# Performance work log

Hardware: AMD Instinct MI355X
Metric: run time of the kernel (lower is better)

Reference implementation:

```python
import jax, jax.numpy as jnp
import numpy as np

IN_DIM, UNITS, OUT_DIM = 128, 256, 8
DENSITY = 0.5  # 1 - sparsity_level
B, T = 256, 512


def _ncp_dims():
    Nm = OUT_DIM
    Nc = max(int(0.4 * (UNITS - Nm)), 1)   # command neurons (AutoNCP rule)
    Ni = UNITS - Nm - Nc                    # inter neurons
    return Ni, Nc, Nm


def _fanout_mask(rng, n_src, n_dst, fanout):
    # each source connects to `fanout` distinct random destinations
    idx = np.argsort(rng.random((n_src, n_dst)), axis=1)[:, :fanout]
    m = np.zeros((n_src, n_dst), dtype=np.int32)
    m[np.arange(n_src)[:, None], idx] = 1
    return m


def setup_inputs() -> dict:
    key = jax.random.key(0)
    rng = np.random.default_rng(22222)
    Ni, Nc, Nm = _ncp_dims()
    s_fan = max(int(Ni * DENSITY), 1)       # sensory fanout
    i_fan = max(int(Nc * DENSITY), 1)       # inter fanout
    m_fanin = max(int(Nc * DENSITY), 1)     # motor fanin
    M_si = _fanout_mask(rng, IN_DIM, Ni, s_fan)      # sensory -> inter
    M_ic = _fanout_mask(rng, Ni, Nc, i_fan)          # inter -> command
    M_cm = _fanout_mask(rng, Nm, Nc, m_fanin).T      # command -> motor (fanin per motor)

    def layer_mask(M_in, hid):
        # WiredCfCCell: concat input sparsity with dense ones for the recurrent block, then transpose
        return np.concatenate([M_in, np.ones((hid, hid), np.int32)], axis=0).T

    masks = [layer_mask(M_si, Ni), layer_mask(M_ic, Nc), layer_mask(M_cm, Nm)]
    dims = [(IN_DIM, Ni), (Ni, Nc), (Nc, Nm)]
    inp = {}
    for l, (fin, hid) in enumerate(dims):
        cat = fin + hid
        scale = 1.0 / np.sqrt(cat)
        for nm in ("w1", "w2", "wa", "wb"):
            inp[f"{nm}_{l}"] = jnp.asarray(rng.normal(0.0, scale, (hid, cat)).astype(np.float32))
        for nm in ("b1", "b2", "ba", "bb"):
            inp[f"{nm}_{l}"] = jnp.zeros((hid,), jnp.float32)
        inp[f"m{l}"] = jnp.asarray(masks[l])  # int32, constant sparsity mask
    k1, k2 = jax.random.split(key)
    inp["x"] = jax.random.normal(k1, (B, T, IN_DIM), jnp.float32)
    inp["dt"] = jax.random.uniform(k2, (1,), jnp.float32, 0.5, 1.5)
    return inp


def _cfc_cell(xh, w1, b1, w2, b2, wa, ba, wb, bb, m, ts):
    # CfCCell, mode='default', no backbone, sparsity mask on ff1/ff2 weights
    mf = m.astype(w1.dtype)
    ff1 = jnp.tanh(xh @ (w1 * mf).T + b1)
    ff2 = jnp.tanh(xh @ (w2 * mf).T + b2)
    t_interp = jax.nn.sigmoid((xh @ wa.T + ba) * ts + (xh @ wb.T + bb))
    return ff1 * (1.0 - t_interp) + t_interp * ff2


def _forward(x, dt, params, masks):
    Ni, Nc, Nm = _ncp_dims()
    ts = dt[0]
    h0 = jnp.zeros((x.shape[0], Ni), x.dtype)
    h1 = jnp.zeros((x.shape[0], Nc), x.dtype)
    h2 = jnp.zeros((x.shape[0], Nm), x.dtype)
    p0, p1, p2 = params

    def step(carry, xt):
        h0, h1, h2 = carry
        nh0 = _cfc_cell(jnp.concatenate([xt, h0], 1), *p0, masks[0], ts)
        nh1 = _cfc_cell(jnp.concatenate([nh0, h1], 1), *p1, masks[1], ts)
        nh2 = _cfc_cell(jnp.concatenate([nh1, h2], 1), *p2, masks[2], ts)
        return (nh0, nh1, nh2), nh2

    (h0, h1, h2), ys = jax.lax.scan(step, (h0, h1, h2), jnp.swapaxes(x, 0, 1))
    y = jnp.tanh(jnp.swapaxes(ys, 0, 1))          # (B, T, OUT_DIM), tanh output saturation
    h_out = jnp.concatenate([h0, h1, h2], axis=1)  # (B, units)
    return y, h_out


def reference(x, dt,
              w1_0, b1_0, w2_0, b2_0, wa_0, ba_0, wb_0, bb_0, m0,
              w1_1, b1_1, w2_1, b2_1, wa_1, ba_1, wb_1, bb_1, m1,
              w1_2, b1_2, w2_2, b2_2, wa_2, ba_2, wb_2, bb_2, m2):
    params = ((w1_0, b1_0, w2_0, b2_0, wa_0, ba_0, wb_0, bb_0),
              (w1_1, b1_1, w2_1, b2_1, wa_1, ba_1, wb_1, bb_1),
              (w1_2, b1_2, w2_2, b2_2, wa_2, ba_2, wb_2, bb_2))
    return _forward(x, dt, params, (m0, m1, m2))
```

## Files before the change

kernel.cpp:

```cpp
#include <hip/hip_runtime.h>
#include <cmath>


typedef _Float16 f16;
typedef f16 h4 __attribute__((ext_vector_type(4)));
typedef f16 h8 __attribute__((ext_vector_type(8)));
typedef float f4 __attribute__((ext_vector_type(4)));

#define MFMA(a, b, c) __builtin_amdgcn_mfma_f32_16x16x32_f16(a, b, c, 0, 0, 0)
#define RAW_BAR() asm volatile("s_waitcnt lgkmcnt(0)\n\ts_barrier" ::: "memory")

constexpr int IN_DIM = 128, Ni = 149, Nc = 99, Nm = 8;
constexpr int CAT0 = 277, CAT1 = 248, CAT2 = 107;
constexpr int Bsz = 256, Tsz = 512;
constexpr int TC = 64, NCH = 8, NBT = 16;
constexpr int NSUB = NCH * 4;
constexpr int NT0 = 30, NT1 = 21;
constexpr int S0 = 168, S2 = 136;
constexpr int NXWG1 = 64;
constexpr int NXWG0 = 128;
constexpr size_t XU0C = (size_t)TC * NBT * NT0 * 256;
constexpr size_t NH0C = (size_t)TC * NBT * 2560;
constexpr size_t XU1C = (size_t)TC * NBT * NT1 * 256;
constexpr size_t H0S_HALVES = (size_t)NBT * 16 * S0;
constexpr size_t H12S_HALVES = (size_t)NBT * 2 * 16 * S2;
constexpr size_t YOFF = (size_t)Bsz * Tsz * 8;
constexpr float L2E = 1.4426950408889634f;

constexpr int OFF_X0 = 0;
constexpr int OFF_R0 = 7680;
constexpr int OFF_X1 = 17280;
constexpr int OFF_R12A = 24000;
constexpr int OFF_R12B = 29376;
constexpr int NFRAG = 30144;

constexpr int CSTRIDE = 16;
constexpr int C_X0 = 0, C_R0S = 8, C_X1S = 40, C_R12S = 72;
constexpr int NCNT = 104 * CSTRIDE;

__device__ inline float rcpf_(float x) { return __builtin_amdgcn_rcpf(x); }
__device__ __forceinline__ float exp2p_(float x) {
#if __has_builtin(__builtin_amdgcn_exp2f)
  return __builtin_amdgcn_exp2f(x);
#else
  return exp2f(x);
#endif
}
__device__ __forceinline__ float cfc_h(float a0, float a1, float a2) {
  float e0 = exp2p_(a0), e1 = exp2p_(a1), e2 = exp2p_(a2);
  float pa = 1.f + e0, ma = 1.f - e0;
  float pb = 1.f + e1, mb = 1.f - e1;
  float pc = 1.f + e2;
  float num = fmaf(ma * pb, e2, mb * pa);
  return num * rcpf_(pa * pb * pc);
}
__device__ __forceinline__ float tanhp_(float x) {
  float e = exp2p_(-2.f * L2E * x);
  return (1.f - e) * rcpf_(1.f + e);
}

__device__ __forceinline__ void spin_relaxed(int* p, int target) {
  if (threadIdx.x == 0) {
    long it = 0;
    while (__hip_atomic_load(p, __ATOMIC_RELAXED, __HIP_MEMORY_SCOPE_AGENT) <
               target &&
           ++it < (1L << 22))
      __builtin_amdgcn_s_sleep(4);
  }
  __syncthreads();
}
__device__ __forceinline__ void spin_acq(int* p, int target) {
  spin_relaxed(p, target);
  __builtin_amdgcn_fence(__ATOMIC_ACQUIRE, "agent");
}
__device__ __forceinline__ void sig_relaxed(int* p) {
  __syncthreads();
  if (threadIdx.x == 0)
    __hip_atomic_fetch_add(p, 1, __ATOMIC_RELAXED, __HIP_MEMORY_SCOPE_AGENT);
}
__device__ __forceinline__ void sig_rel(int* p) {
  __syncthreads();
  if (threadIdx.x == 0)
    __hip_atomic_fetch_add(p, 1, __ATOMIC_RELEASE, __HIP_MEMORY_SCOPE_AGENT);
}

__device__ __forceinline__ void store_short_sc(f16* p, f16 v) {
  unsigned u = (unsigned)__builtin_bit_cast(unsigned short, v);
  asm volatile("global_store_short %0, %1, off sc0 sc1" ::"v"(
                   (unsigned long long)p),
               "v"(u)
               : "memory");
}
__device__ __forceinline__ void load_A5_sc(const f16* base, h8 (&A)[5]) {
  unsigned long long b = (unsigned long long)base;
  asm volatile(
      "global_load_dwordx4 %0, %5, off sc0 sc1\n\t"
      "global_load_dwordx4 %1, %5, off offset:64 sc0 sc1\n\t"
      "global_load_dwordx4 %2, %5, off offset:128 sc0 sc1\n\t"
      "global_load_dwordx4 %3, %5, off offset:192 sc0 sc1\n\t"
      "global_load_dwordx4 %4, %5, off offset:256 sc0 sc1\n\t"
      "s_waitcnt vmcnt(0)"
      : "=&v"(A[0]), "=&v"(A[1]), "=&v"(A[2]), "=&v"(A[3]), "=&v"(A[4])
      : "v"(b)
      : "memory");
}

__global__ __launch_bounds__(256) void pack_kernel(
    const float* __restrict__ w1_0, const float* __restrict__ w2_0,
    const float* __restrict__ wa_0, const float* __restrict__ wb_0,
    const int* __restrict__ m0,
    const float* __restrict__ w1_1, const float* __restrict__ w2_1,
    const float* __restrict__ wa_1, const float* __restrict__ wb_1,
    const int* __restrict__ m1,
    const float* __restrict__ w1_2, const float* __restrict__ w2_2,
    const float* __restrict__ wa_2, const float* __restrict__ wb_2,
    const int* __restrict__ m2, const float* __restrict__ dtp,
    f16* __restrict__ PK, int* __restrict__ CNT) {
  if (blockIdx.x == 0)
    for (int i = threadIdx.x; i < NCNT; i += 256)
      __hip_atomic_store(&CNT[i], 0, __ATOMIC_RELAXED, __HIP_MEMORY_SCOPE_AGENT);
  int idx = blockIdx.x * 256 + threadIdx.x;
  if (idx >= NFRAG) return;
  int lane = idx & 63, col = lane & 15, q = lane >> 4;
  float ts = dtp[0];
  const float* Wa = nullptr;
  const float* Wb = nullptr;
  const int* M = nullptr;
  int ld, n, nmax, k0, kmax;
  int mat;
  if (idx < OFF_R0) {
    int p = idx >> 6;
    mat = p / 40; int nt = (p >> 2) % 10, kt = p & 3;
    ld = CAT0; n = nt * 16 + col; nmax = Ni; k0 = kt * 32 + q * 8; kmax = IN_DIM;
    if (mat == 0) { Wa = w1_0; M = m0; }
    else if (mat == 1) { Wa = w2_0; M = m0; }
    else { Wa = wa_0; Wb = wb_0; }
  } else if (idx < OFF_X1) {
    int p = (idx - OFF_R0) >> 6;
    int g = p / 15; mat = (p / 5) % 3; int kt = p % 5;
    ld = CAT0; n = g * 16 + col; nmax = Ni; k0 = IN_DIM + kt * 32 + q * 8; kmax = CAT0;
    if (mat == 0) Wa = w1_0;
    else if (mat == 1) Wa = w2_0;
    else { Wa = wa_0; Wb = wb_0; }
  } else if (idx < OFF_R12A) {
    int p = (idx - OFF_X1) >> 6;
    mat = p / 35; int nt = (p / 5) % 7, kt = p % 5;
    ld = CAT1; n = nt * 16 + col; nmax = Nc; k0 = kt * 32 + q * 8; kmax = Ni;
    if (mat == 0) { Wa = w1_1; M = m1; }
    else if (mat == 1) { Wa = w2_1; M = m1; }
    else { Wa = wa_1; Wb = wb_1; }
  } else if (idx < OFF_R12B) {
    int p = (idx - OFF_R12A) >> 6;
    int wv = p / 12; mat = (p / 4) % 3; int kt = p & 3;
    ld = CAT1; n = wv * 16 + col; nmax = Nc; k0 = Ni + kt * 32 + q * 8; kmax = CAT1;
    if (mat == 0) Wa = w1_1;
    else if (mat == 1) Wa = w2_1;
    else { Wa = wa_1; Wb = wb_1; }
  } else {
    int p = (idx - OFF_R12B) >> 6;
    mat = p / 4; int kt = p & 3;
    ld = CAT2; n = col; nmax = Nm; k0 = kt * 32 + q * 8; kmax = CAT2;
    if (mat == 0) { Wa = w1_2; M = m2; }
    else if (mat == 1) { Wa = w2_2; M = m2; }
    else { Wa = wa_2; Wb = wb_2; }
  }
  h8 r;
#pragma unroll
  for (int j = 0; j < 8; j++) {
    int k = k0 + j;
    float v = 0.f;
    if (n < nmax && k < kmax) {
      if (mat < 2) {
        v = Wa[(size_t)n * ld + k];
        if (M) v *= (float)M[(size_t)n * ld + k];
        v *= -2.f * L2E;
      } else {
        v = -L2E * (ts * Wa[(size_t)n * ld + k] + Wb[(size_t)n * ld + k]);
      }
    }
    r[j] = (f16)v;
  }
  ((h8*)PK)[idx] = r;
}

__device__ __forceinline__ void r0_step(
    const f16* br, f16* bw, const f16* __restrict__ XU0, f16* __restrict__ NH0,
    float* __restrict__ out, const h8 (&Bf)[3][5], h4 (&xu)[3],
    int t, int tload, int bt, int g, int lane, int col, int q, int n, bool last) {
  h8 A[5];
#pragma unroll
  for (int kt = 0; kt < 5; kt++)
    A[kt] = *(const h8*)(br + col * S0 + kt * 32 + q * 8);
  f4 acc0 = {(float)xu[0][0], (float)xu[0][1], (float)xu[0][2], (float)xu[0][3]};
  f4 acc1 = {(float)xu[1][0], (float)xu[1][1], (float)xu[1][2], (float)xu[1][3]};
  f4 acc2 = {(float)xu[2][0], (float)xu[2][1], (float)xu[2][2], (float)xu[2][3]};
  size_t mtl = (size_t)tload * NBT + bt;
#pragma unroll
  for (int mat = 0; mat < 3; mat++)
    xu[mat] = *(const h4*)(XU0 + (mtl * NT0 + mat * 10 + g) * 256 + lane * 4);
#pragma unroll
  for (int kt = 0; kt < 5; kt++) {
    acc0 = MFMA(A[kt], Bf[0][kt], acc0);
    acc1 = MFMA(A[kt], Bf[1][kt], acc1);
    acc2 = MFMA(A[kt], Bf[2][kt], acc2);
  }
  int mt = t * NBT + bt;
  f16* nh = NH0 + (size_t)mt * 2560;
#pragma unroll
  for (int r = 0; r < 4; r++) {
    int m = q * 4 + r;
    float h = cfc_h(acc0[r], acc1[r], acc2[r]);
    f16 h16 = (f16)h;
    bw[m * S0 + n] = h16;
    store_short_sc(nh + (size_t)m * 160 + n, h16);
    if (last && n < Ni) out[YOFF + (size_t)(bt * 16 + m) * 256 + n] = h;
  }
}

__device__ __forceinline__ void r12l1_step(
    const f16* br, f16* bw, const f16* __restrict__ XU1, float* __restrict__ out,
    const h8 (&Bf)[3][4], h4 (&xu)[3],
    int tload, int bt, int w, int lane, int col, int q, int n, bool last) {
  h8 A[4];
#pragma unroll
  for (int kt = 0; kt < 4; kt++)
    A[kt] = *(const h8*)(br + col * S2 + kt * 32 + q * 8);
  f4 acc0 = {(float)xu[0][0], (float)xu[0][1], (float)xu[0][2], (float)xu[0][3]};
  f4 acc1 = {(float)xu[1][0], (float)xu[1][1], (float)xu[1][2], (float)xu[1][3]};
  f4 acc2 = {(float)xu[2][0], (float)xu[2][1], (float)xu[2][2], (float)xu[2][3]};
  size_t mtl = (size_t)tload * NBT + bt;
#pragma unroll
  for (int mat = 0; mat < 3; mat++)
    xu[mat] = *(const h4*)(XU1 + (mtl * NT1 + mat * 7 + w) * 256 + lane * 4);
#pragma unroll
  for (int kt = 0; kt < 4; kt++) {
    acc0 = MFMA(A[kt], Bf[0][kt], acc0);
    acc1 = MFMA(A[kt], Bf[1][kt], acc1);
    acc2 = MFMA(A[kt], Bf[2][kt], acc2);
  }
#pragma unroll
  for (int r = 0; r < 4; r++) {
    int m = q * 4 + r;
    float h = cfc_h(acc0[r], acc1[r], acc2[r]);
    if (n < Nc) {
      bw[m * S2 + n] = (f16)h;
      if (last) out[YOFF + (size_t)(bt * 16 + m) * 256 + Ni + n] = h;
    }
  }
}

__device__ __forceinline__ void r12l2_step(
    const f16* rb, f16* wb, float* __restrict__ out, const h8 (&Bf)[3][4],
    float bn0, float bn1, float bn2, int tg, int bt, int col, int q, bool last) {
  h8 A[4];
#pragma unroll
  for (int kt = 0; kt < 4; kt++)
    A[kt] = *(const h8*)(rb + col * S2 + kt * 32 + q * 8);
  f4 acc0 = {bn0, bn0, bn0, bn0};
  f4 acc1 = {bn1, bn1, bn1, bn1};
  f4 acc2 = {bn2, bn2, bn2, bn2};
#pragma unroll
  for (int kt = 0; kt < 4; kt++) {
    acc0 = MFMA(A[kt], Bf[0][kt], acc0);
    acc1 = MFMA(A[kt], Bf[1][kt], acc1);
    acc2 = MFMA(A[kt], Bf[2][kt], acc2);
  }
#pragma unroll
  for (int r = 0; r < 4; r++) {
    int m = q * 4 + r;
    float h = cfc_h(acc0[r], acc1[r], acc2[r]);
    if (col < Nm) {
      out[((size_t)(bt * 16 + m) * Tsz + tg) * 8 + col] = tanhp_(h);
      wb[m * S2 + Nc + col] = (f16)h;
      if (last) out[YOFF + (size_t)(bt * 16 + m) * 256 + Ni + Nc + col] = h;
    }
  }
}

__global__ __launch_bounds__(640) void R_kernel(
    const h8* __restrict__ pk,
    const float* __restrict__ b1_0, const float* __restrict__ b2_0,
    const float* __restrict__ ba_0, const float* __restrict__ bb_0,
    const float* __restrict__ b1_1, const float* __restrict__ b2_1,
    const float* __restrict__ ba_1, const float* __restrict__ bb_1,
    const float* __restrict__ c1, const float* __restrict__ c2,
    const float* __restrict__ ca, const float* __restrict__ cb,
    const float* __restrict__ dtp, const float* __restrict__ x,
    f16* __restrict__ XU0, f16* __restrict__ NH0, f16* __restrict__ XU1,
    f16* __restrict__ H0S, f16* __restrict__ H12S,
    int* __restrict__ CNT, float* __restrict__ out, int c) {
  __shared__ __align__(16) char smem[10752];
  int tid = threadIdx.x;
  int g = tid >> 6, lane = tid & 63, col = lane & 15, q = lane >> 4;
  int wg = blockIdx.x;
  float ts = dtp[0];

  if (wg < NBT) {
    if (c < 0 || c >= NCH) return;
    spin_relaxed(&CNT[(C_X0 + c) * CSTRIDE], NXWG0);
    if (c >= 2)
      spin_relaxed(&CNT[(C_X1S + 4 * (c - 2) + 3) * CSTRIDE], NBT);
    const f16* XU0r = XU0 + (size_t)(c & 1) * XU0C;
    f16* NH0w = NH0 + (size_t)(c & 1) * NH0C;
    f16(*buf)[16 * S0] = (f16(*)[16 * S0])smem;
    int bt = wg;
    int n = g * 16 + col;
    h8 Bf[3][5];
#pragma unroll
    for (int mat = 0; mat < 3; mat++)
#pragma unroll
      for (int kt = 0; kt < 5; kt++)
        Bf[mat][kt] = pk[OFF_R0 + ((g * 3 + mat) * 5 + kt) * 64 + lane];

    for (int idx = tid; idx < 16 * S0; idx += 640) {
      buf[0][idx] = (c == 0) ? (f16)0.f : H0S[(size_t)bt * 16 * S0 + idx];
      buf[1][idx] = (f16)0.f;
    }
    __syncthreads();

    h4 xu0[3], xu1[3], xu2[3], xu3[3];
#pragma unroll
    for (int mat = 0; mat < 3; mat++) {
      xu0[mat] = *(const h4*)(XU0r + ((size_t)(0 * NBT + bt) * NT0 + mat * 10 + g) * 256 + lane * 4);
      xu1[mat] = *(const h4*)(XU0r + ((size_t)(1 * NBT + bt) * NT0 + mat * 10 + g) * 256 + lane * 4);
      xu2[mat] = *(const h4*)(XU0r + ((size_t)(2 * NBT + bt) * NT0 + mat * 10 + g) * 256 + lane * 4);
      xu3[mat] = *(const h4*)(XU0r + ((size_t)(3 * NBT + bt) * NT0 + mat * 10 + g) * 256 + lane * 4);
    }

    for (int t = 0; t < TC; t += 4) {
      r0_step(buf[0], buf[1], XU0r, NH0w, out, Bf, xu0, t, (t + 4 < TC) ? t + 4 : t,
              bt, g, lane, col, q, n, false);
      RAW_BAR();
      r0_step(buf[1], buf[0], XU0r, NH0w, out, Bf, xu1, t + 1,
              (t + 5 < TC) ? t + 5 : t + 1, bt, g, lane, col, q, n, false);
      RAW_BAR();
      r0_step(buf[0], buf[1], XU0r, NH0w, out, Bf, xu2, t + 2,
              (t + 6 < TC) ? t + 6 : t + 2, bt, g, lane, col, q, n, false);
      RAW_BAR();
      bool lastD = (c == NCH - 1) && (t + 3 == TC - 1);
      r0_step(buf[1], buf[0], XU0r, NH0w, out, Bf, xu3, t + 3,
              (t + 7 < TC) ? t + 7 : t + 3, bt, g, lane, col, q, n, lastD);
      RAW_BAR();
      if ((t & 12) == 12)
        sig_relaxed(&CNT[(C_R0S + 4 * c + (t >> 4)) * CSTRIDE]);
    }
    for (int idx = tid; idx < 16 * S0; idx += 640)
      H0S[(size_t)bt * 16 * S0 + idx] = buf[0][idx];

  } else if (wg < 2 * NBT) {
    int Glo = 4 * c - 2; if (Glo < 0) Glo = 0;
    int Ghi = 4 * c + 1; if (Ghi > NSUB - 1) Ghi = NSUB - 1;
    if (Glo > Ghi || c < 0) return;
    f16(*buf)[16 * S2] = (f16(*)[16 * S2])smem;
    int bt = wg - NBT;
    int w = g;
    int n = w * 16 + col;
    h8 Bf[3][4];
    float bn0 = 0.f, bn1 = 0.f, bn2 = 0.f;
    if (w < 7) {
#pragma unroll
      for (int mat = 0; mat < 3; mat++)
#pragma unroll
        for (int kt = 0; kt < 4; kt++)
          Bf[mat][kt] = pk[OFF_R12A + ((w * 3 + mat) * 4 + kt) * 64 + lane];
    } else if (w == 7) {
#pragma unroll
      for (int mat = 0; mat < 3; mat++)
#pragma unroll
        for (int kt = 0; kt < 4; kt++)
          Bf[mat][kt] = pk[OFF_R12B + (mat * 4 + kt) * 64 + lane];
      bn0 = (col < Nm) ? -2.f * L2E * c1[col] : 0.f;
      bn1 = (col < Nm) ? -2.f * L2E * c2[col] : 0.f;
      bn2 = (col < Nm) ? -L2E * (ts * ca[col] + cb[col]) : 0.f;
    }
    for (int idx = tid; idx < 2 * 16 * S2; idx += 640)
      ((f16*)buf)[idx] = (Glo == 0) ? (f16)0.f : H12S[(size_t)bt * 2 * 16 * S2 + idx];
    __syncthreads();

    for (int G = Glo; G <= Ghi; ++G) {
      int m = G >> 2, t0 = (G & 3) * 16;
      spin_acq(&CNT[(C_X1S + G) * CSTRIDE], NBT);
      const f16* XU1r = XU1 + (size_t)(m & 1) * XU1C;
      h4 xuA[3], xuB[3];
      if (w < 7) {
#pragma unroll
        for (int mat = 0; mat < 3; mat++) {
          xuA[mat] = *(const h4*)(XU1r + ((size_t)(t0 * NBT + bt) * NT1 + mat * 7 + w) * 256 + lane * 4);
          xuB[mat] = *(const h4*)(XU1r +
                                  ((size_t)((t0 + 1) * NBT + bt) * NT1 + mat * 7 + w) * 256 + lane * 4);
        }
      }
      for (int t = t0; t < t0 + 16; t += 2) {
        if (w < 7) {
          int tlA = (t + 2 < t0 + 16) ? t + 2 : t;
          r12l1_step(buf[0], buf[1], XU1r, out, Bf, xuA, tlA, bt, w, lane, col, q, n,
                     false);
        }
        RAW_BAR();
        if (w == 7)
          r12l2_step(buf[1], buf[0], out, Bf, bn0, bn1, bn2, m * TC + t, bt, col, q,
                     false);
        if (w < 7) {
          int tlB = (t + 3 < t0 + 16) ? t + 3 : t + 1;
          bool lastB = (m == NCH - 1) && (t + 1 == TC - 1);
          r12l1_step(buf[1], buf[0], XU1r, out, Bf, xuB, tlB, bt, w, lane, col, q, n,
                     lastB);
        }
        RAW_BAR();
        if (w == 7)
          r12l2_step(buf[0], buf[1], out, Bf, bn0, bn1, bn2, m * TC + t + 1, bt, col,
                     q, (m == NCH - 1) && (t + 1 == TC - 1));
      }
      sig_relaxed(&CNT[(C_R12S + G) * CSTRIDE]);
    }
    for (int idx = tid; idx < 2 * 16 * S2; idx += 640)
      H12S[(size_t)bt * 2 * 16 * S2 + idx] = ((f16*)buf)[idx];

  } else if (wg < 2 * NBT + NXWG1) {
    int bx = wg - 2 * NBT;
    int k = bx >> 4;
    int m = (k == 3) ? c - 1 : c;
    if (m < 0 || m >= NCH) return;
    int G = 4 * m + k;
    int w = g;
    int n = w * 16 + col;
    h8 Bf[3][5];
    float bias[3] = {0.f, 0.f, 0.f};
    if (w < 7) {
#pragma unroll
      for (int mat = 0; mat < 3; mat++)
#pragma unroll
        for (int kt = 0; kt < 5; kt++)
          Bf[mat][kt] = pk[OFF_X1 + (mat * 35 + w * 5 + kt) * 64 + lane];
      bias[0] = (n < Nc) ? -2.f * L2E * b1_1[n] : 0.f;
      bias[1] = (n < Nc) ? -2.f * L2E * b2_1[n] : 0.f;
      bias[2] = (n < Nc) ? -L2E * (ts * ba_1[n] + bb_1[n]) : 0.f;
    }
    spin_relaxed(&CNT[(C_R0S + G) * CSTRIDE], NBT);
    if (m >= 2)
      spin_relaxed(&CNT[(C_R12S + 4 * (m - 2) + 3) * CSTRIDE], NBT);
    const f16* NH0r = NH0 + (size_t)(m & 1) * NH0C;
    f16* XU1w = XU1 + (size_t)(m & 1) * XU1C;
    if (w < 7) {
      for (int i = 0; i < 16; i++) {
        int mt = bx * 16 + i;
        const f16* base = NH0r + (size_t)mt * 2560 + col * 160 + q * 8;
        h8 A[5];
        load_A5_sc(base, A);
#pragma unroll
        for (int mat = 0; mat < 3; mat++) {
          float b = bias[mat];
          f4 acc = {b, b, b, b};
#pragma unroll
          for (int kt = 0; kt < 5; kt++) acc = MFMA(A[kt], Bf[mat][kt], acc);
          h4 o;
#pragma unroll
          for (int rr = 0; rr < 4; rr++) o[rr] = (f16)acc[rr];
          *(h4*)(XU1w + ((size_t)mt * NT1 + mat * 7 + w) * 256 + lane * 4) = o;
        }
      }
    }
    sig_rel(&CNT[(C_X1S + G) * CSTRIDE]);

  } else {
    int cn = c + 1;
    if (cn >= NCH) return;
    if (cn >= 2)
      spin_relaxed(&CNT[(C_R0S + 4 * (cn - 2) + 3) * CSTRIDE], NBT);
    f16* XU0w = XU0 + (size_t)(cn & 1) * XU0C;
    f16* stg = (f16*)smem;
    int bx = wg - 2 * NBT - NXWG1;
    int w = g;
    int n = w * 16 + col;
    h8 Bx[3][4];
    float bias[3];
#pragma unroll
    for (int mat = 0; mat < 3; mat++)
#pragma unroll
      for (int kt = 0; kt < 4; kt++)
        Bx[mat][kt] = pk[OFF_X0 + ((mat * 10 + w) * 4 + kt) * 64 + lane];
    bias[0] = (n < Ni) ? -2.f * L2E * b1_0[n] : 0.f;
    bias[1] = (n < Ni) ? -2.f * L2E * b2_0[n] : 0.f;
    bias[2] = (n < Ni) ? -L2E * (ts * ba_0[n] + bb_0[n]) : 0.f;
    for (int i = 0; i < (TC * NBT) / NXWG0; i++) {
      int mt = bx * ((TC * NBT) / NXWG0) + i;
      int tl = mt >> 4, bt = mt & 15;
      int tg = cn * TC + tl;
      if (tid < 256) {
        int sr = tid >> 4, sc = (tid & 15) * 8;
        const float* xp = x + ((size_t)(bt * 16 + sr) * Tsz + tg) * IN_DIM + sc;
        h8 hv;
#pragma unroll
        for (int j = 0; j < 8; j++) hv[j] = (f16)xp[j];
        *(h8*)(stg + sr * 136 + sc) = hv;
      }
      __syncthreads();
      h8 A[4];
#pragma unroll
      for (int kt = 0; kt < 4; kt++)
        A[kt] = *(const h8*)(stg + col * 136 + kt * 32 + q * 8);
#pragma unroll
      for (int mat = 0; mat < 3; mat++) {
        float b = bias[mat];
        f4 acc = {b, b, b, b};
#pragma unroll
        for (int kt = 0; kt < 4; kt++) acc = MFMA(A[kt], Bx[mat][kt], acc);
        h4 o;
#pragma unroll
        for (int rr = 0; rr < 4; rr++) o[rr] = (f16)acc[rr];
        *(h4*)(XU0w + ((size_t)mt * NT0 + mat * 10 + w) * 256 + lane * 4) = o;
      }
      __syncthreads();
    }
    sig_relaxed(&CNT[(C_X0 + cn) * CSTRIDE]);
  }
}

extern "C" void kernel_launch(void* const* d_in, const int* in_sizes, int n_in,
                              void* d_out, int out_size, void* d_ws, size_t ws_size,
                              hipStream_t stream) {
  const float* w1_0 = (const float*)d_in[0];
  const float* w2_0 = (const float*)d_in[1];
  const float* wa_0 = (const float*)d_in[2];
  const float* wb_0 = (const float*)d_in[3];
  const float* b1_0 = (const float*)d_in[4];
  const float* b2_0 = (const float*)d_in[5];
  const float* ba_0 = (const float*)d_in[6];
  const float* bb_0 = (const float*)d_in[7];
  const int* m0 = (const int*)d_in[8];
  const float* w1_1 = (const float*)d_in[9];
  const float* w2_1 = (const float*)d_in[10];
  const float* wa_1 = (const float*)d_in[11];
  const float* wb_1 = (const float*)d_in[12];
  const float* b1_1 = (const float*)d_in[13];
  const float* b2_1 = (const float*)d_in[14];
  const float* ba_1 = (const float*)d_in[15];
  const float* bb_1 = (const float*)d_in[16];
  const int* m1 = (const int*)d_in[17];
  const float* w1_2 = (const float*)d_in[18];
  const float* w2_2 = (const float*)d_in[19];
  const float* wa_2 = (const float*)d_in[20];
  const float* wb_2 = (const float*)d_in[21];
  const float* c1 = (const float*)d_in[22];
  const float* c2 = (const float*)d_in[23];
  const float* ca = (const float*)d_in[24];
  const float* cb = (const float*)d_in[25];
  const int* m2 = (const int*)d_in[26];
  const float* x = (const float*)d_in[27];
  const float* dt = (const float*)d_in[28];
  float* out = (float*)d_out;

  f16* XU0 = (f16*)d_ws;
  f16* NH0 = XU0 + 2 * XU0C;
  f16* XU1 = NH0 + 2 * NH0C;
  f16* H0S = XU1 + 2 * XU1C;
  f16* H12S = H0S + H0S_HALVES;
  f16* PK = H12S + H12S_HALVES;
  int* CNT = (int*)(PK + (size_t)NFRAG * 8);
  const h8* pk = (const h8*)PK;

  hipMemsetAsync(CNT, 0, NCNT * sizeof(int), stream);

  pack_kernel<<<(NFRAG + 255) / 256, 256, 0, stream>>>(
      w1_0, w2_0, wa_0, wb_0, m0, w1_1, w2_1, wa_1, wb_1, m1,
      w1_2, w2_2, wa_2, wb_2, m2, dt, PK, CNT);

  for (int c = -1; c <= NCH; c++)
    R_kernel<<<2 * NBT + NXWG1 + NXWG0, 640, 0, stream>>>(
        pk, b1_0, b2_0, ba_0, bb_0, b1_1, b2_1, ba_1, bb_1,
        c1, c2, ca, cb, dt, x, XU0, NH0, XU1, H0S, H12S, CNT, out, c);
}
```

Before: 706.0 us.

## Fold weight packing into first R_kernel launch and drop trailing launch

Removes the separate pack_kernel launch by having the c==-1 launch of R_kernel pack weight fragments, synchronize all workgroups through a grid-wide counter, then compute chunk 0's input projection across all workgroups. The final c==NCH launch is removed by moving its remaining work (the last chunk's layer-1 input projection and recurrent tail) into the c==NCH-1 launch, with extra spin waits on existing counters. This cuts two kernel launches and spreads the first chunk's projection across more workgroups. It relies on all 240 workgroups being co-resident for the grid-wide spin, which could deadlock if occupancy doesn't allow it.

Result: slower. 725.4 us (+2.7%).

```diff
diff --git a/kernel.cpp b/kernel.cpp
--- a/kernel.cpp
+++ b/kernel.cpp
@@ -19,6 +19,7 @@
 constexpr int S0 = 168, S2 = 136;
 constexpr int NXWG1 = 64;
 constexpr int NXWG0 = 128;
+constexpr int NWGALL = 2 * NBT + NXWG1 + NXWG0;
 constexpr size_t XU0C = (size_t)TC * NBT * NT0 * 256;
 constexpr size_t NH0C = (size_t)TC * NBT * 2560;
 constexpr size_t XU1C = (size_t)TC * NBT * NT1 * 256;
@@ -35,8 +36,8 @@
 constexpr int NFRAG = 30144;
 
 constexpr int CSTRIDE = 16;
-constexpr int C_X0 = 0, C_R0S = 8, C_X1S = 40, C_R12S = 72;
-constexpr int NCNT = 104 * CSTRIDE;
+constexpr int C_X0 = 0, C_R0S = 8, C_X1S = 40, C_R12S = 72, C_PK = 104;
+constexpr int NCNT = 105 * CSTRIDE;
 
 __device__ inline float rcpf_(float x) { return __builtin_amdgcn_rcpf(x); }
 __device__ __forceinline__ float exp2p_(float x) {
@@ -105,7 +106,8 @@
       : "memory");
 }
 
-__global__ __launch_bounds__(256) void pack_kernel(
+__device__ __forceinline__ void pack_one(
+    int idx,
     const float* __restrict__ w1_0, const float* __restrict__ w2_0,
     const float* __restrict__ wa_0, const float* __restrict__ wb_0,
     const int* __restrict__ m0,
@@ -114,15 +116,8 @@
     const int* __restrict__ m1,
     const float* __restrict__ w1_2, const float* __restrict__ w2_2,
     const float* __restrict__ wa_2, const float* __restrict__ wb_2,
-    const int* __restrict__ m2, const float* __restrict__ dtp,
-    f16* __restrict__ PK, int* __restrict__ CNT) {
-  if (blockIdx.x == 0)
-    for (int i = threadIdx.x; i < NCNT; i += 256)
-      __hip_atomic_store(&CNT[i], 0, __ATOMIC_RELAXED, __HIP_MEMORY_SCOPE_AGENT);
-  int idx = blockIdx.x * 256 + threadIdx.x;
-  if (idx >= NFRAG) return;
+    const int* __restrict__ m2, float ts, f16* __restrict__ PK) {
   int lane = idx & 63, col = lane & 15, q = lane >> 4;
-  float ts = dtp[0];
   const float* Wa = nullptr;
   const float* Wb = nullptr;
   const int* M = nullptr;
@@ -278,7 +273,16 @@
 }
 
 __global__ __launch_bounds__(640) void R_kernel(
-    const h8* __restrict__ pk,
+    f16* __restrict__ PK,
+    const float* __restrict__ w1_0, const float* __restrict__ w2_0,
+    const float* __restrict__ wa_0, const float* __restrict__ wb_0,
+    const int* __restrict__ m0,
+    const float* __restrict__ w1_1, const float* __restrict__ w2_1,
+    const float* __restrict__ wa_1, const float* __restrict__ wb_1,
+    const int* __restrict__ m1,
+    const float* __restrict__ w1_2, const float* __restrict__ w2_2,
+    const float* __restrict__ wa_2, const float* __restrict__ wb_2,
+    const int* __restrict__ m2,
     const float* __restrict__ b1_0, const float* __restrict__ b2_0,
     const float* __restrict__ ba_0, const float* __restrict__ bb_0,
     const float* __restrict__ b1_1, const float* __restrict__ b2_1,
@@ -294,10 +298,62 @@
   int g = tid >> 6, lane = tid & 63, col = lane & 15, q = lane >> 4;
   int wg = blockIdx.x;
   float ts = dtp[0];
+  const h8* pk = (const h8*)PK;
+
+  if (c == -1) {
+    int idx = wg * 640 + tid;
+    if (idx < NFRAG)
+      pack_one(idx, w1_0, w2_0, wa_0, wb_0, m0, w1_1, w2_1, wa_1, wb_1, m1,
+               w1_2, w2_2, wa_2, wb_2, m2, ts, PK);
+    sig_rel(&CNT[C_PK * CSTRIDE]);
+    spin_acq(&CNT[C_PK * CSTRIDE], NWGALL);
+    f16* stg = (f16*)smem;
+    int w = g, n = w * 16 + col;
+    h8 Bx[3][4];
+    float bias[3];
+#pragma unroll
+    for (int mat = 0; mat < 3; mat++)
+#pragma unroll
+      for (int kt = 0; kt < 4; kt++)
+        Bx[mat][kt] = pk[OFF_X0 + ((mat * 10 + w) * 4 + kt) * 64 + lane];
+    bias[0] = (n < Ni) ? -2.f * L2E * b1_0[n] : 0.f;
+    bias[1] = (n < Ni) ? -2.f * L2E * b2_0[n] : 0.f;
+    bias[2] = (n < Ni) ? -L2E * (ts * ba_0[n] + bb_0[n]) : 0.f;
+    for (int mt = wg; mt < TC * NBT; mt += NWGALL) {
+      int tl = mt >> 4, bt = mt & 15;
+      int tg = tl;
+      if (tid < 256) {
+        int sr = tid >> 4, sc = (tid & 15) * 8;
+        const float* xp = x + ((size_t)(bt * 16 + sr) * Tsz + tg) * IN_DIM + sc;
+        h8 hv;
+#pragma unroll
+        for (int j = 0; j < 8; j++) hv[j] = (f16)xp[j];
+        *(h8*)(stg + sr * 136 + sc) = hv;
+      }
+      __syncthreads();
+      h8 A[4];
+#pragma unroll
+      for (int kt = 0; kt < 4; kt++)
+        A[kt] = *(const h8*)(stg + col * 136 + kt * 32 + q * 8);
+#pragma unroll
+      for (int mat = 0; mat < 3; mat++) {
+        float b = bias[mat];
+        f4 acc = {b, b, b, b};
+#pragma unroll
+        for (int kt = 0; kt < 4; kt++) acc = MFMA(A[kt], Bx[mat][kt], acc);
+        h4 o;
+#pragma unroll
+        for (int rr = 0; rr < 4; rr++) o[rr] = (f16)acc[rr];
+        *(h4*)(XU0 + ((size_t)mt * NT0 + mat * 10 + w) * 256 + lane * 4) = o;
+      }
+      __syncthreads();
+    }
+    sig_relaxed(&CNT[(C_X0 + 0) * CSTRIDE]);
+    return;
+  }
 
   if (wg < NBT) {
-    if (c < 0 || c >= NCH) return;
-    spin_relaxed(&CNT[(C_X0 + c) * CSTRIDE], NXWG0);
+    spin_relaxed(&CNT[(C_X0 + c) * CSTRIDE], c == 0 ? NWGALL : NXWG0);
     if (c >= 2)
       spin_relaxed(&CNT[(C_X1S + 4 * (c - 2) + 3) * CSTRIDE], NBT);
     const f16* XU0r = XU0 + (size_t)(c & 1) * XU0C;
@@ -349,8 +405,7 @@
 
   } else if (wg < 2 * NBT) {
     int Glo = 4 * c - 2; if (Glo < 0) Glo = 0;
-    int Ghi = 4 * c + 1; if (Ghi > NSUB - 1) Ghi = NSUB - 1;
-    if (Glo > Ghi || c < 0) return;
+    int Ghi = (c == NCH - 1) ? (NSUB - 1) : (4 * c + 1);
     f16(*buf)[16 * S2] = (f16(*)[16 * S2])smem;
     int bt = wg - NBT;
     int w = g;
@@ -464,12 +519,54 @@
 
   } else {
     int cn = c + 1;
-    if (cn >= NCH) return;
+    int bx = wg - 2 * NBT - NXWG1;
+    if (cn >= NCH) {
+      if (c != NCH - 1 || bx >= NBT) return;
+      int w = g;
+      int n = w * 16 + col;
+      h8 Bf[3][5];
+      float bias[3] = {0.f, 0.f, 0.f};
+      if (w < 7) {
+#pragma unroll
+        for (int mat = 0; mat < 3; mat++)
+#pragma unroll
+          for (int kt = 0; kt < 5; kt++)
+            Bf[mat][kt] = pk[OFF_X1 + (mat * 35 + w * 5 + kt) * 64 + lane];
+        bias[0] = (n < Nc) ? -2.f * L2E * b1_1[n] : 0.f;
+        bias[1] = (n < Nc) ? -2.f * L2E * b2_1[n] : 0.f;
+        bias[2] = (n < Nc) ? -L2E * (ts * ba_1[n] + bb_1[n]) : 0.f;
+      }
+      spin_relaxed(&CNT[(C_R0S + NSUB - 1) * CSTRIDE], NBT);
+      spin_relaxed(&CNT[(C_R12S + 4 * (NCH - 3) + 3) * CSTRIDE], NBT);
+      const f16* NH0r = NH0 + (size_t)((NCH - 1) & 1) * NH0C;
+      f16* XU1w = XU1 + (size_t)((NCH - 1) & 1) * XU1C;
+      int tt = 48 + bx;
+      if (w < 7) {
+        for (int i = 0; i < 16; i++) {
+          int mt = tt * 16 + i;
+          const f16* base = NH0r + (size_t)mt * 2560 + col * 160 + q * 8;
+          h8 A[5];
+          load_A5_sc(base, A);
+#pragma unroll
+          for (int mat = 0; mat < 3; mat++) {
+            float b = bias[mat];
+            f4 acc = {b, b, b, b};
+#pragma unroll
+            for (int kt = 0; kt < 5; kt++) acc = MFMA(A[kt], Bf[mat][kt], acc);
+            h4 o;
+#pragma unroll
+            for (int rr = 0; rr < 4; rr++) o[rr] = (f16)acc[rr];
+            *(h4*)(XU1w + ((size_t)mt * NT1 + mat * 7 + w) * 256 + lane * 4) = o;
+          }
+        }
+      }
+      sig_rel(&CNT[(C_X1S + NSUB - 1) * CSTRIDE]);
+      return;
+    }
     if (cn >= 2)
       spin_relaxed(&CNT[(C_R0S + 4 * (cn - 2) + 3) * CSTRIDE], NBT);
     f16* XU0w = XU0 + (size_t)(cn & 1) * XU0C;
     f16* stg = (f16*)smem;
-    int bx = wg - 2 * NBT - NXWG1;
     int w = g;
     int n = w * 16 + col;
     h8 Bx[3][4];
@@ -557,16 +654,13 @@
   f16* H12S = H0S + H0S_HALVES;
   f16* PK = H12S + H12S_HALVES;
   int* CNT = (int*)(PK + (size_t)NFRAG * 8);
-  const h8* pk = (const h8*)PK;
 
   hipMemsetAsync(CNT, 0, NCNT * sizeof(int), stream);
 
-  pack_kernel<<<(NFRAG + 255) / 256, 256, 0, stream>>>(
-      w1_0, w2_0, wa_0, wb_0, m0, w1_1, w2_1, wa_1, wb_1, m1,
-      w1_2, w2_2, wa_2, wb_2, m2, dt, PK, CNT);
-
-  for (int c = -1; c <= NCH; c++)
-    R_kernel<<<2 * NBT + NXWG1 + NXWG0, 640, 0, stream>>>(
-        pk, b1_0, b2_0, ba_0, bb_0, b1_1, b2_1, ba_1, bb_1,
+  for (int c = -1; c < NCH; c++)
+    R_kernel<<<NWGALL, 640, 0, stream>>>(
+        PK, w1_0, w2_0, wa_0, wb_0, m0, w1_1, w2_1, wa_1, wb_1, m1,
+        w1_2, w2_2, wa_2, wb_2, m2,
+        b1_0, b2_0, ba_0, bb_0, b1_1, b2_1, ba_1, bb_1,
         c1, c2, ca, cb, dt, x, XU0, NH0, XU1, H0S, H12S, CNT, out, c);
 }
```
